# Kernel tuning notes

Measured on AMD Instinct MI355X. Metric: run time of the kernel, lower is better.

The kernel has to match this reference:

```python
import jax, jax.numpy as jnp
import numpy as np

N_ROWS = 16384
INP_UNITS = 8192
OUT_UNITS = 128
NNZ = 1_048_576


def setup_inputs() -> dict:
    key = jax.random.key(0)
    k1, k2, k3, k4 = jax.random.split(key, 4)
    values = jax.random.normal(k1, (NNZ,), dtype=jnp.float32)
    w = jax.random.normal(k2, (INP_UNITS, OUT_UNITS), dtype=jnp.float32)
    # COO indices, rows sorted as in a canonical tf.SparseTensor
    rows = jnp.sort(jax.random.randint(k3, (NNZ,), 0, N_ROWS, dtype=jnp.int32)).astype(jnp.int64)
    cols = jax.random.randint(k4, (NNZ,), 0, INP_UNITS, dtype=jnp.int32).astype(jnp.int64)
    return {"values": values, "w": w, "rows": rows, "cols": cols, "n_rows": N_ROWS}


def reference(values, w, rows, cols, n_rows):
    # sparse (COO) x dense matmul: out[r, :] = sum_{k: rows[k]==r} values[k] * w[cols[k], :]
    contrib = values[:, None] * w[cols]  # [nnz, out_units]
    return jax.ops.segment_sum(contrib, rows, num_segments=n_rows)
```

## Files before the change

kernel.cpp:

```cpp
#include <hip/hip_runtime.h>

#define OUT_UNITS 128

__global__ void build_row_starts(const int* __restrict__ rows,
                                 int* __restrict__ row_start,
                                 int nnz, int n_rows) {
    int k = blockIdx.x * blockDim.x + threadIdx.x;
    if (k >= nnz) return;
    int cur = rows[k];
    if (k == 0) {
        for (int r = 0; r <= cur; ++r) row_start[r] = 0;
    } else {
        int prev = rows[k - 1];
        for (int r = prev + 1; r <= cur; ++r) row_start[r] = k;
    }
    if (k == nnz - 1) {
        for (int r = cur + 1; r <= n_rows; ++r) row_start[r] = nnz;
    }
}

__global__ __launch_bounds__(256)
void spmm_row_wave(const float* __restrict__ vals,
                   const float* __restrict__ w,
                   const int* __restrict__ cols,
                   const int* __restrict__ row_start,
                   float* __restrict__ out,
                   int n_rows) {
    __shared__ int2 cvbuf[4][64];

    const int wave = __builtin_amdgcn_readfirstlane((int)(threadIdx.x >> 6));
    const int lane = threadIdx.x & 63;
    const int r    = blockIdx.x * 4 + wave;
    if (r >= n_rows) return;

    const int start = row_start[r];
    const int end   = row_start[r + 1];
    const int half  = lane >> 5;
    const int sub   = lane & 31;
    const float4* __restrict__ w4 = (const float4*)w;
    int2* cv = cvbuf[wave];

    float4 acc = make_float4(0.f, 0.f, 0.f, 0.f);

    for (int base = start; base < end; base += 64) {
        const int navail = min(64, end - base);
        const int idx = base + min(lane, navail - 1);
        int   c_l = cols[idx];
        float v_l = (lane < navail) ? vals[idx] : 0.f;
        cv[lane] = make_int2(c_l, __float_as_int(v_l));

        const int npair  = (navail + 1) >> 1;
        const int npair4 = (npair + 3) & ~3;

        for (int t = 0; t < npair4; t += 4) {
            int2 p0 = cv[2 * t + 0 + half];
            int2 p1 = cv[2 * t + 2 + half];
            int2 p2 = cv[2 * t + 4 + half];
            int2 p3 = cv[2 * t + 6 + half];
            float4 w0 = w4[((size_t)(unsigned)p0.x << 5) + sub];
            float4 w1 = w4[((size_t)(unsigned)p1.x << 5) + sub];
            float4 w2 = w4[((size_t)(unsigned)p2.x << 5) + sub];
            float4 w3 = w4[((size_t)(unsigned)p3.x << 5) + sub];
            float v0 = __int_as_float(p0.y);
            float v1 = __int_as_float(p1.y);
            float v2 = __int_as_float(p2.y);
            float v3 = __int_as_float(p3.y);
            acc.x = fmaf(v0, w0.x, acc.x); acc.y = fmaf(v0, w0.y, acc.y);
            acc.z = fmaf(v0, w0.z, acc.z); acc.w = fmaf(v0, w0.w, acc.w);
            acc.x = fmaf(v1, w1.x, acc.x); acc.y = fmaf(v1, w1.y, acc.y);
            acc.z = fmaf(v1, w1.z, acc.z); acc.w = fmaf(v1, w1.w, acc.w);
            acc.x = fmaf(v2, w2.x, acc.x); acc.y = fmaf(v2, w2.y, acc.y);
            acc.z = fmaf(v2, w2.z, acc.z); acc.w = fmaf(v2, w2.w, acc.w);
            acc.x = fmaf(v3, w3.x, acc.x); acc.y = fmaf(v3, w3.y, acc.y);
            acc.z = fmaf(v3, w3.z, acc.z); acc.w = fmaf(v3, w3.w, acc.w);
        }
    }

    acc.x += __shfl_xor(acc.x, 32);
    acc.y += __shfl_xor(acc.y, 32);
    acc.z += __shfl_xor(acc.z, 32);
    acc.w += __shfl_xor(acc.w, 32);

    if (half == 0) {
        ((float4*)(out + (size_t)r * OUT_UNITS))[sub] = acc;
    }
}

extern "C" void kernel_launch(void* const* d_in, const int* in_sizes, int n_in,
                              void* d_out, int out_size, void* d_ws, size_t ws_size,
                              hipStream_t stream) {
    const float* vals = (const float*)d_in[0];
    const float* w    = (const float*)d_in[1];
    const int*   rows = (const int*)d_in[2];
    const int*   cols = (const int*)d_in[3];
    float* out = (float*)d_out;

    const int nnz    = in_sizes[0];
    const int n_rows = out_size / OUT_UNITS;

    int* row_start = (int*)d_ws;

    build_row_starts<<<(nnz + 255) / 256, 256, 0, stream>>>(rows, row_start, nnz, n_rows);
    spmm_row_wave<<<(n_rows + 3) / 4, 256, 0, stream>>>(vals, w, cols, row_start, out, n_rows);
}
```

Before: 98.83 us.

## Convert weights to fp16 in prep kernel and gather half-precision rows

Adds a prep kernel that converts the dense weight matrix to fp16 and fuses this with the row-start construction, so the two run as one launch. The SpMM kernel now gathers 256-byte fp16 weight rows, with each lane handling two output columns across the full wave, instead of 512-byte fp32 rows split across half-waves. This roughly halves the gather traffic and removes the cross-half shuffle reduction. The cost is fp16 rounding of the weights, which loosens accuracy, plus an extra pass over the weight matrix on every call.

```diff
diff --git a/kernel.cpp b/kernel.cpp
--- a/kernel.cpp
+++ b/kernel.cpp
@@ -1,27 +1,35 @@
 #include <hip/hip_runtime.h>
+#include <hip/hip_fp16.h>
 
 #define OUT_UNITS 128
 
-__global__ void build_row_starts(const int* __restrict__ rows,
-                                 int* __restrict__ row_start,
-                                 int nnz, int n_rows) {
-    int k = blockIdx.x * blockDim.x + threadIdx.x;
-    if (k >= nnz) return;
-    int cur = rows[k];
-    if (k == 0) {
-        for (int r = 0; r <= cur; ++r) row_start[r] = 0;
-    } else {
-        int prev = rows[k - 1];
-        for (int r = prev + 1; r <= cur; ++r) row_start[r] = k;
+__global__ void prep(const float4* __restrict__ w4, uint2* __restrict__ wh, int n4,
+                     const int* __restrict__ rows, int* __restrict__ row_start,
+                     int nnz, int n_rows) {
+    int i = blockIdx.x * blockDim.x + threadIdx.x;
+    if (i < n4) {
+        float4 f = w4[i];
+        __half2 h01 = __floats2half2_rn(f.x, f.y);
+        __half2 h23 = __floats2half2_rn(f.z, f.w);
+        wh[i] = make_uint2(*(unsigned*)&h01, *(unsigned*)&h23);
     }
-    if (k == nnz - 1) {
-        for (int r = cur + 1; r <= n_rows; ++r) row_start[r] = nnz;
+    if (i < nnz) {
+        int cur = rows[i];
+        if (i == 0) {
+            for (int r = 0; r <= cur; ++r) row_start[r] = 0;
+        } else {
+            int prev = rows[i - 1];
+            for (int r = prev + 1; r <= cur; ++r) row_start[r] = i;
+        }
+        if (i == nnz - 1) {
+            for (int r = cur + 1; r <= n_rows; ++r) row_start[r] = nnz;
+        }
     }
 }
 
-__global__ __launch_bounds__(256)
+__global__ __launch_bounds__(256, 4)
 void spmm_row_wave(const float* __restrict__ vals,
-                   const float* __restrict__ w,
+                   const __half* __restrict__ wh,
                    const int* __restrict__ cols,
                    const int* __restrict__ row_start,
                    float* __restrict__ out,
@@ -35,12 +43,11 @@
 
     const int start = row_start[r];
     const int end   = row_start[r + 1];
-    const int half  = lane >> 5;
-    const int sub   = lane & 31;
-    const float4* __restrict__ w4 = (const float4*)w;
+    const char* __restrict__ whb = (const char*)wh;
+    const int loff = lane << 2;
     int2* cv = cvbuf[wave];
 
-    float4 acc = make_float4(0.f, 0.f, 0.f, 0.f);
+    float2 acc = make_float2(0.f, 0.f);
 
     for (int base = start; base < end; base += 64) {
         const int navail = min(64, end - base);
@@ -49,41 +56,37 @@
         float v_l = (lane < navail) ? vals[idx] : 0.f;
         cv[lane] = make_int2(c_l, __float_as_int(v_l));
 
-        const int npair  = (navail + 1) >> 1;
-        const int npair4 = (npair + 3) & ~3;
+        const int n4 = (navail + 3) & ~3;
 
-        for (int t = 0; t < npair4; t += 4) {
-            int2 p0 = cv[2 * t + 0 + half];
-            int2 p1 = cv[2 * t + 2 + half];
-            int2 p2 = cv[2 * t + 4 + half];
-            int2 p3 = cv[2 * t + 6 + half];
-            float4 w0 = w4[((size_t)(unsigned)p0.x << 5) + sub];
-            float4 w1 = w4[((size_t)(unsigned)p1.x << 5) + sub];
-            float4 w2 = w4[((size_t)(unsigned)p2.x << 5) + sub];
-            float4 w3 = w4[((size_t)(unsigned)p3.x << 5) + sub];
+        for (int t = 0; t < n4; t += 4) {
+            int2 p0 = cv[t + 0];
+            int2 p1 = cv[t + 1];
+            int2 p2 = cv[t + 2];
+            int2 p3 = cv[t + 3];
+            unsigned q0 = *(const unsigned*)(whb + (((size_t)(unsigned)p0.x) << 8) + loff);
+            unsigned q1 = *(const unsigned*)(whb + (((size_t)(unsigned)p1.x) << 8) + loff);
+            unsigned q2 = *(const unsigned*)(whb + (((size_t)(unsigned)p2.x) << 8) + loff);
+            unsigned q3 = *(const unsigned*)(whb + (((size_t)(unsigned)p3.x) << 8) + loff);
+            __half2 h0 = *(__half2*)&q0;
+            __half2 h1 = *(__half2*)&q1;
+            __half2 h2 = *(__half2*)&q2;
+            __half2 h3 = *(__half2*)&q3;
             float v0 = __int_as_float(p0.y);
             float v1 = __int_as_float(p1.y);
             float v2 = __int_as_float(p2.y);
             float v3 = __int_as_float(p3.y);
-            acc.x = fmaf(v0, w0.x, acc.x); acc.y = fmaf(v0, w0.y, acc.y);
-            acc.z = fmaf(v0, w0.z, acc.z); acc.w = fmaf(v0, w0.w, acc.w);
-            acc.x = fmaf(v1, w1.x, acc.x); acc.y = fmaf(v1, w1.y, acc.y);
-            acc.z = fmaf(v1, w1.z, acc.z); acc.w = fmaf(v1, w1.w, acc.w);
-            acc.x = fmaf(v2, w2.x, acc.x); acc.y = fmaf(v2, w2.y, acc.y);
-            acc.z = fmaf(v2, w2.z, acc.z); acc.w = fmaf(v2, w2.w, acc.w);
-            acc.x = fmaf(v3, w3.x, acc.x); acc.y = fmaf(v3, w3.y, acc.y);
-            acc.z = fmaf(v3, w3.z, acc.z); acc.w = fmaf(v3, w3.w, acc.w);
+            acc.x = fmaf(v0, __half2float(h0.x), acc.x);
+            acc.y = fmaf(v0, __half2float(h0.y), acc.y);
+            acc.x = fmaf(v1, __half2float(h1.x), acc.x);
+            acc.y = fmaf(v1, __half2float(h1.y), acc.y);
+            acc.x = fmaf(v2, __half2float(h2.x), acc.x);
+            acc.y = fmaf(v2, __half2float(h2.y), acc.y);
+            acc.x = fmaf(v3, __half2float(h3.x), acc.x);
+            acc.y = fmaf(v3, __half2float(h3.y), acc.y);
         }
     }
 
-    acc.x += __shfl_xor(acc.x, 32);
-    acc.y += __shfl_xor(acc.y, 32);
-    acc.z += __shfl_xor(acc.z, 32);
-    acc.w += __shfl_xor(acc.w, 32);
-
-    if (half == 0) {
-        ((float4*)(out + (size_t)r * OUT_UNITS))[sub] = acc;
-    }
+    ((float2*)(out + (size_t)r * OUT_UNITS))[lane] = acc;
 }
 
 extern "C" void kernel_launch(void* const* d_in, const int* in_sizes, int n_in,
@@ -97,9 +100,14 @@
 
     const int nnz    = in_sizes[0];
     const int n_rows = out_size / OUT_UNITS;
+    const int w_n    = in_sizes[1];
+    const int n4     = w_n / 4;
 
-    int* row_start = (int*)d_ws;
+    int*    row_start = (int*)d_ws;
+    __half* wh        = (__half*)((char*)d_ws + (128 << 10));
 
-    build_row_starts<<<(nnz + 255) / 256, 256, 0, stream>>>(rows, row_start, nnz, n_rows);
-    spmm_row_wave<<<(n_rows + 3) / 4, 256, 0, stream>>>(vals, w, cols, row_start, out, n_rows);
+    const int prep_threads = (nnz > n4) ? nnz : n4;
+    prep<<<(prep_threads + 255) / 256, 256, 0, stream>>>(
+        (const float4*)w, (uint2*)wh, n4, rows, row_start, nnz, n_rows);
+    spmm_row_wave<<<(n_rows + 3) / 4, 256, 0, stream>>>(vals, wh, cols, row_start, out, n_rows);
 }
```

Result: faster. 91.31 us (-7.6%).
